# Kernel tuning notes

Measured on AMD Instinct MI355X. Metric: run time of the kernel, lower is better.

## Reference

```python
import jax, jax.numpy as jnp
import numpy as np

EMBED_DIM = 1024
NUM_HEADS = 16
HEAD_DIM = EMBED_DIM // NUM_HEADS


def setup_inputs() -> dict:
    key = jax.random.key(0)
    ks = jax.random.split(key, 11)
    B, S, E = 4, 2048, EMBED_DIM
    s = 1.0 / np.sqrt(E)
    return {
        "q": jax.random.normal(ks[0], (B, S, E), jnp.float32),
        "k": jax.random.normal(ks[1], (B, S, E), jnp.float32),
        "v": jax.random.normal(ks[2], (B, S, E), jnp.float32),
        "Wq": jax.random.uniform(ks[3], (E, E), jnp.float32, -s, s),
        "bq": jax.random.uniform(ks[4], (E,), jnp.float32, -s, s),
        "Wk": jax.random.uniform(ks[5], (E, E), jnp.float32, -s, s),
        "bk": jax.random.uniform(ks[6], (E,), jnp.float32, -s, s),
        "Wv": jax.random.uniform(ks[7], (E, E), jnp.float32, -s, s),
        "bv": jax.random.uniform(ks[8], (E,), jnp.float32, -s, s),
        "Wo": jax.random.uniform(ks[9], (E, E), jnp.float32, -s, s),
        "bo": jax.random.uniform(ks[10], (E,), jnp.float32, -s, s),
    }


def _split_heads(x):
    B, S, E = x.shape
    return x.reshape(B, S, NUM_HEADS, HEAD_DIM).transpose(0, 2, 1, 3)  # [B,H,S,D]


def reference(q, k, v, Wq, bq, Wk, bk, Wv, bv, Wo, bo):
    # torch Linear: x @ W.T + b
    Q = _split_heads(q @ Wq.T + bq)
    K = _split_heads(k @ Wk.T + bk)
    V = _split_heads(v @ Wv.T + bv)
    scale = 1.0 / jnp.sqrt(jnp.float32(HEAD_DIM))
    scores = jnp.einsum("bhqd,bhkd->bhqk", Q, K) * scale  # [B,H,S,S]
    weights = jax.nn.softmax(scores, axis=-1)
    ctx = jnp.einsum("bhqk,bhkd->bhqd", weights, V)
    B, H, S, D = ctx.shape
    merged = ctx.transpose(0, 2, 1, 3).reshape(B, S, H * D)
    out = merged @ Wo.T + bo
    return out, weights
```

## Files before the change

### kernel.cpp

```cpp
#include <hip/hip_runtime.h>
#include <hip/hip_bf16.h>

typedef __bf16 bf16x8 __attribute__((ext_vector_type(8)));
typedef float f32x4 __attribute__((ext_vector_type(4)));

constexpr size_t XQ_OFF = 0;
constexpr size_t WQ_OFF = 25165824;
constexpr size_t Q_OFF  = 29360128;
constexpr size_t KK_OFF = 37748736;
constexpr size_t VT_OFF = 46137344;
constexpr size_t CTX_OFF= 54525952;

__device__ __forceinline__ void gload16(const void* g, void* s) {
    __builtin_amdgcn_global_load_lds((__attribute__((address_space(1))) void*)g,
                                     (__attribute__((address_space(3))) void*)s, 16, 0, 0);
}
#define WAIT_VM0()   asm volatile("s_waitcnt vmcnt(0)" ::: "memory")
#define WAIT_VM4()   asm volatile("s_waitcnt vmcnt(4)" ::: "memory")
#define WAIT_VM8()   asm volatile("s_waitcnt vmcnt(8)" ::: "memory")
#define WAIT_LGKM0() asm volatile("s_waitcnt lgkmcnt(0)" ::: "memory")
#define BAR()        __builtin_amdgcn_s_barrier()

__global__ __launch_bounds__(256) void convert_k(
    const float* __restrict__ q, const float* __restrict__ k, const float* __restrict__ v,
    const float* __restrict__ Wq, const float* __restrict__ Wk, const float* __restrict__ Wv,
    const float* __restrict__ Wo, __bf16* __restrict__ ws) {
    int id = blockIdx.x * 256 + threadIdx.x;
    const int NX = 1048576;
    const int NW = 131072;
    const float* src; size_t dst; int local;
    if (id < 3 * NX) {
        int z = id / NX; local = id - z * NX;
        src = (z == 0) ? q : ((z == 1) ? k : v);
        dst = XQ_OFF + (size_t)z * 8388608;
    } else {
        int i2 = id - 3 * NX;
        int z = i2 / NW; local = i2 - z * NW;
        src = (z == 0) ? Wq : ((z == 1) ? Wk : ((z == 2) ? Wv : Wo));
        dst = WQ_OFF + (size_t)z * 1048576;
    }
    const float4* s4 = (const float4*)(src + (size_t)local * 8);
    float4 a = s4[0], b = s4[1];
    bf16x8 o;
    o[0]=(__bf16)a.x; o[1]=(__bf16)a.y; o[2]=(__bf16)a.z; o[3]=(__bf16)a.w;
    o[4]=(__bf16)b.x; o[5]=(__bf16)b.y; o[6]=(__bf16)b.z; o[7]=(__bf16)b.w;
    *(bf16x8*)(ws + dst + (size_t)local * 8) = o;
}

template<int MODE>
__global__ __launch_bounds__(256) void gemm_k(
    __bf16* __restrict__ ws,
    const float* __restrict__ bq, const float* __restrict__ bk,
    const float* __restrict__ bv, const float* __restrict__ bo,
    float* __restrict__ out) {
    const int K = 1024;
    unsigned n = blockIdx.x + 64u * (blockIdx.y + 8u * blockIdx.z);
    unsigned cpx = (MODE == 0) ? 192u : 64u;
    unsigned m_ = (n & 7u) * cpx + (n >> 3);
    unsigned bx = m_ & 63u;
    unsigned rest = m_ >> 6;
    unsigned by = rest & 7u;
    unsigned bz = rest >> 3;

    int z = (int)bz;
    const __bf16* A; const __bf16* Bm; const float* bias;
    if (MODE == 0) {
        A    = ws + XQ_OFF + (size_t)z * 8388608;
        Bm   = ws + WQ_OFF + (size_t)z * 1048576;
        bias = (z == 0) ? bq : ((z == 1) ? bk : bv);
    } else {
        A    = ws + CTX_OFF;
        Bm   = ws + WQ_OFF + (size_t)3 * 1048576;
        bias = bo;
    }
    int row0 = (int)bx * 128, col0 = (int)by * 128;
    __shared__ __align__(16) __bf16 As[2][128 * 32];
    __shared__ __align__(16) __bf16 Bs[2][128 * 32];
    int t = threadIdx.x, lane = t & 63, w = t >> 6;
    int wr = w >> 1, wc = w & 1;
    f32x4 acc[4][4];
#pragma unroll
    for (int i = 0; i < 4; ++i)
#pragma unroll
        for (int j = 0; j < 4; ++j) acc[i][j] = (f32x4){0.f, 0.f, 0.f, 0.f};

    auto stage = [&](int buf, int kt) {
#pragma unroll
        for (int i = 0; i < 2; ++i) {
            int e = ((i * 4 + w) * 64 + lane) * 8;
            int r = e >> 5, c = e & 31;
            gload16(A  + (size_t)(row0 + r) * K + kt + c, &As[buf][e]);
            gload16(Bm + (size_t)(col0 + r) * K + kt + c, &Bs[buf][e]);
        }
    };

    stage(0, 0);
    int cur = 0;
    for (int kt = 0; kt < K; kt += 32) {
        bool nx = kt + 32 < K;
        if (nx) { stage(cur ^ 1, kt + 32); WAIT_VM4(); }
        else    { WAIT_VM0(); }
        BAR();
        const __bf16* Ac = As[cur];
        const __bf16* Bc = Bs[cur];
        bf16x8 af[4], bfr[4];
#pragma unroll
        for (int f = 0; f < 4; ++f) {
            af[f]  = *(const bf16x8*)&Ac[(wr * 64 + f * 16 + (lane & 15)) * 32 + (lane >> 4) * 8];
            bfr[f] = *(const bf16x8*)&Bc[(wc * 64 + f * 16 + (lane & 15)) * 32 + (lane >> 4) * 8];
        }
#pragma unroll
        for (int fr = 0; fr < 4; ++fr)
#pragma unroll
            for (int fc = 0; fc < 4; ++fc)
                acc[fr][fc] = __builtin_amdgcn_mfma_f32_16x16x32_bf16(af[fr], bfr[fc], acc[fr][fc], 0, 0, 0);
        WAIT_LGKM0();
        BAR();
        cur ^= 1;
    }

    if (MODE == 0) {
        __bf16* dqk = ws + Q_OFF + (size_t)z * 8388608;
        __bf16* dvt = ws + VT_OFF;
#pragma unroll
        for (int fr = 0; fr < 4; ++fr)
#pragma unroll
            for (int fc = 0; fc < 4; ++fc)
#pragma unroll
                for (int r = 0; r < 4; ++r) {
                    int m = row0 + wr * 64 + fr * 16 + ((lane >> 4) << 2) + r;
                    int nn = col0 + wc * 64 + fc * 16 + (lane & 15);
                    float val = acc[fr][fc][r] + bias[nn];
                    int bb = m >> 11, s = m & 2047, h = nn >> 6, d = nn & 63;
                    size_t bh = (size_t)bb * 16 + h;
                    if (z < 2) dqk[bh * 131072 + (size_t)s * 64 + d] = (__bf16)val;
                    else       dvt[bh * 131072 + (size_t)d * 2048 + s] = (__bf16)val;
                }
    } else {
#pragma unroll
        for (int fr = 0; fr < 4; ++fr)
#pragma unroll
            for (int fc = 0; fc < 4; ++fc)
#pragma unroll
                for (int r = 0; r < 4; ++r) {
                    int m = row0 + wr * 64 + fr * 16 + ((lane >> 4) << 2) + r;
                    int nn = col0 + wc * 64 + fc * 16 + (lane & 15);
                    out[(size_t)m * 1024 + nn] = acc[fr][fc][r] + bias[nn];
                }
    }
}

__global__ __launch_bounds__(512) void rowsum_k(const __bf16* __restrict__ ws,
                                                float* __restrict__ rs_out) {
    unsigned n = blockIdx.x + 8u * blockIdx.y;
    unsigned m = (n & 7u) * 64u + (n >> 3);
    int bh = (int)(m >> 3);
    int q0 = (int)(m & 7u) * 256;
    const __bf16* Qb = ws + Q_OFF  + (size_t)bh * 131072;
    const __bf16* Kb = ws + KK_OFF + (size_t)bh * 131072;
    __shared__ __align__(16) __bf16 Ks[2][64 * 64];
    int t = threadIdx.x, lane = t & 63, w = t >> 6, g = lane >> 4;
    const float SCALE = 0.125f;

    bf16x8 aq[2][2];
#pragma unroll
    for (int f = 0; f < 2; ++f) {
        int qr = q0 + w * 32 + f * 16 + (lane & 15);
        aq[f][0] = *(const bf16x8*)&Qb[(size_t)qr * 64 + g * 8];
        aq[f][1] = *(const bf16x8*)&Qb[(size_t)qr * 64 + 32 + g * 8];
    }

    { int r = t >> 3, c8 = t & 7;
      gload16(Kb + (size_t)r * 64 + ((c8 ^ (r & 7)) << 3), &Ks[0][t * 8]); }
    WAIT_VM0(); BAR();

    float rs[8] = {0.f,0.f,0.f,0.f,0.f,0.f,0.f,0.f};
    int cur = 0;
    for (int kt = 0; kt < 2048; kt += 64) {
        bool nx = kt < 1984;
        if (nx) {
            int r = t >> 3, c8 = t & 7;
            gload16(Kb + (size_t)(kt + 64 + r) * 64 + ((c8 ^ (r & 7)) << 3), &Ks[cur ^ 1][t * 8]);
        }
        const __bf16* Kc = Ks[cur];
        __builtin_amdgcn_s_setprio(1);
#pragma unroll
        for (int kc = 0; kc < 4; ++kc) {
            int krow = kc * 16 + (lane & 15);
            bf16x8 b0 = *(const bf16x8*)((const char*)Kc + krow * 128 + ((g * 16) ^ ((krow & 7) << 4)));
            bf16x8 b1 = *(const bf16x8*)((const char*)Kc + krow * 128 + (((4 + g) * 16) ^ ((krow & 7) << 4)));
#pragma unroll
            for (int f = 0; f < 2; ++f) {
                f32x4 s = (f32x4){0.f, 0.f, 0.f, 0.f};
                s = __builtin_amdgcn_mfma_f32_16x16x32_bf16(aq[f][0], b0, s, 0, 0, 0);
                s = __builtin_amdgcn_mfma_f32_16x16x32_bf16(aq[f][1], b1, s, 0, 0, 0);
#pragma unroll
                for (int r4 = 0; r4 < 4; ++r4) rs[f * 4 + r4] += __expf(s[r4] * SCALE);
            }
        }
        __builtin_amdgcn_s_setprio(0);
        WAIT_LGKM0();
        if (nx) WAIT_VM0();
        BAR();
        cur ^= 1;
    }
#pragma unroll
    for (int msk = 1; msk < 16; msk <<= 1)
#pragma unroll
        for (int i = 0; i < 8; ++i) rs[i] += __shfl_xor(rs[i], msk);
    if ((lane & 15) == 0) {
#pragma unroll
        for (int f = 0; f < 2; ++f)
#pragma unroll
            for (int r4 = 0; r4 < 4; ++r4)
                rs_out[(size_t)bh * 2048 + q0 + w * 32 + f * 16 + g * 4 + r4] = rs[f * 4 + r4];
    }
}

__global__ __launch_bounds__(512) void attnw_k(const __bf16* __restrict__ ws,
                                               const float* __restrict__ rsf,
                                               __bf16* __restrict__ wsw,
                                               float* __restrict__ wout) {
    unsigned n = blockIdx.x + 8u * blockIdx.y;
    unsigned m = (n & 7u) * 64u + (n >> 3);
    int bh = (int)(m >> 3);
    int q0 = (int)(m & 7u) * 256;

    const __bf16* Qb = ws + Q_OFF  + (size_t)bh * 131072;
    const __bf16* Kb = ws + KK_OFF + (size_t)bh * 131072;
    const __bf16* Vb = ws + VT_OFF + (size_t)bh * 131072;
    __bf16* ctx = wsw + CTX_OFF;

    int t = threadIdx.x, lane = t & 63, w = t >> 6, g = lane >> 4;
    __shared__ __align__(16) __bf16 QP[256 * 64];
    __shared__ __align__(16) __bf16 Ks[2][64 * 64];
    __shared__ __align__(16) __bf16 Vts[2][64 * 64];
    const float SCALE = 0.125f;

    float rinv[8];
#pragma unroll
    for (int f = 0; f < 2; ++f)
#pragma unroll
        for (int r4 = 0; r4 < 4; ++r4)
            rinv[f * 4 + r4] = 1.f / rsf[(size_t)bh * 2048 + q0 + w * 32 + f * 16 + g * 4 + r4];

#pragma unroll
    for (int i = 0; i < 4; ++i) {
        int ch = t + 512 * i, r = ch >> 3, c8 = ch & 7;
        gload16(Qb + (size_t)(q0 + r) * 64 + ((c8 ^ (r & 7)) << 3), &QP[ch * 8]);
    }
    WAIT_VM0(); BAR();
    bf16x8 aq[2][2];
#pragma unroll
    for (int f = 0; f < 2; ++f) {
        int qrow = w * 32 + f * 16 + (lane & 15);
        aq[f][0] = *(const bf16x8*)((const char*)QP + qrow * 128 + ((g * 16) ^ ((qrow & 7) << 4)));
        aq[f][1] = *(const bf16x8*)((const char*)QP + qrow * 128 + (((4 + g) * 16) ^ ((qrow & 7) << 4)));
    }
    WAIT_LGKM0(); BAR();

    { int r = t >> 3, c8 = t & 7;
      gload16(Kb + (size_t)r * 64   + ((c8 ^ (r & 7)) << 3), &Ks[0][t * 8]);
      gload16(Vb + (size_t)r * 2048 + ((c8 ^ (r & 7)) << 3), &Vts[0][t * 8]); }
    WAIT_VM0(); BAR();

    f32x4 cacc[2][4];
#pragma unroll
    for (int f = 0; f < 2; ++f)
#pragma unroll
        for (int dc = 0; dc < 4; ++dc) cacc[f][dc] = (f32x4){0.f, 0.f, 0.f, 0.f};

    int cur = 0;
    for (int kt = 0; kt < 2048; kt += 64) {
        bool nx = kt < 1984;
        if (nx) {
            int r = t >> 3, c8 = t & 7;
            gload16(Kb + (size_t)(kt + 64 + r) * 64 + ((c8 ^ (r & 7)) << 3), &Ks[cur ^ 1][t * 8]);
            gload16(Vb + (size_t)r * 2048 + (kt + 64) + ((c8 ^ (r & 7)) << 3), &Vts[cur ^ 1][t * 8]);
        }
        const __bf16* Kc = Ks[cur];
        const __bf16* Vc = Vts[cur];
        __builtin_amdgcn_s_setprio(1);
#pragma unroll
        for (int kc = 0; kc < 4; ++kc) {
            int krow = kc * 16 + (lane & 15);
            bf16x8 b0 = *(const bf16x8*)((const char*)Kc + krow * 128 + ((g * 16) ^ ((krow & 7) << 4)));
            bf16x8 b1 = *(const bf16x8*)((const char*)Kc + krow * 128 + (((4 + g) * 16) ^ ((krow & 7) << 4)));
#pragma unroll
            for (int f = 0; f < 2; ++f) {
                f32x4 s = (f32x4){0.f, 0.f, 0.f, 0.f};
                s = __builtin_amdgcn_mfma_f32_16x16x32_bf16(aq[f][0], b0, s, 0, 0, 0);
                s = __builtin_amdgcn_mfma_f32_16x16x32_bf16(aq[f][1], b1, s, 0, 0, 0);
#pragma unroll
                for (int r4 = 0; r4 < 4; ++r4) {
                    float e = __expf(s[r4] * SCALE) * rinv[f * 4 + r4];
                    int prow = w * 32 + f * 16 + (g << 2) + r4;
                    int pcol = kc * 16 + (lane & 15);
                    *(__bf16*)((char*)QP + prow * 128 + ((pcol * 2) ^ ((prow & 7) << 4))) = (__bf16)e;
                }
            }
        }
        __builtin_amdgcn_s_setprio(0);
        WAIT_LGKM0();
        __builtin_amdgcn_sched_barrier(0);
        BAR();
#pragma unroll
        for (int i = 0; i < 4; ++i) {
            int ch = t + 512 * i, row = ch >> 3, c8 = ch & 7;
            bf16x8 p = *(const bf16x8*)((const char*)QP + row * 128 + ((c8 * 16) ^ ((row & 7) << 4)));
            f32x4 lo = (f32x4){(float)p[0], (float)p[1], (float)p[2], (float)p[3]};
            f32x4 hi = (f32x4){(float)p[4], (float)p[5], (float)p[6], (float)p[7]};
            float* dst = wout + ((size_t)bh * 2048 + q0 + row) * 2048 + kt + c8 * 8;
            *(f32x4*)dst = lo;
            *(f32x4*)(dst + 4) = hi;
        }
        __builtin_amdgcn_s_setprio(1);
#pragma unroll
        for (int ks = 0; ks < 2; ++ks) {
            bf16x8 ap[2];
#pragma unroll
            for (int f = 0; f < 2; ++f) {
                int arow = w * 32 + f * 16 + (lane & 15);
                ap[f] = *(const bf16x8*)((const char*)QP + arow * 128 + ((ks * 64 + g * 16) ^ ((arow & 7) << 4)));
            }
#pragma unroll
            for (int dc = 0; dc < 4; ++dc) {
                int vrow = dc * 16 + (lane & 15);
                bf16x8 bv = *(const bf16x8*)((const char*)Vc + vrow * 128 + ((ks * 64 + g * 16) ^ ((vrow & 7) << 4)));
#pragma unroll
                for (int f = 0; f < 2; ++f)
                    cacc[f][dc] = __builtin_amdgcn_mfma_f32_16x16x32_bf16(ap[f], bv, cacc[f][dc], 0, 0, 0);
            }
        }
        __builtin_amdgcn_s_setprio(0);
        WAIT_LGKM0();
        WAIT_VM8();
        BAR();
        cur ^= 1;
    }

    int bb = bh >> 4, h = bh & 15;
#pragma unroll
    for (int f = 0; f < 2; ++f)
#pragma unroll
        for (int dc = 0; dc < 4; ++dc)
#pragma unroll
            for (int r4 = 0; r4 < 4; ++r4) {
                int qg = q0 + w * 32 + f * 16 + (g << 2) + r4;
                int d = dc * 16 + (lane & 15);
                ctx[((size_t)bb * 2048 + qg) * 1024 + h * 64 + d] = (__bf16)cacc[f][dc][r4];
            }
}

extern "C" void kernel_launch(void* const* d_in, const int* in_sizes, int n_in,
                              void* d_out, int out_size, void* d_ws, size_t ws_size,
                              hipStream_t stream) {
    const float* q  = (const float*)d_in[0];
    const float* k  = (const float*)d_in[1];
    const float* v  = (const float*)d_in[2];
    const float* Wq = (const float*)d_in[3];
    const float* bq = (const float*)d_in[4];
    const float* Wk = (const float*)d_in[5];
    const float* bk = (const float*)d_in[6];
    const float* Wv = (const float*)d_in[7];
    const float* bv = (const float*)d_in[8];
    const float* Wo = (const float*)d_in[9];
    const float* bo = (const float*)d_in[10];
    __bf16* ws = (__bf16*)d_ws;
    float* out  = (float*)d_out;
    float* wout = out + 8388608;
    float* rsum = (float*)d_ws;

    convert_k<<<dim3(14336), dim3(256), 0, stream>>>(q, k, v, Wq, Wk, Wv, Wo, ws);
    gemm_k<0><<<dim3(64, 8, 3), dim3(256), 0, stream>>>(ws, bq, bk, bv, bo, out);
    rowsum_k<<<dim3(8, 64), dim3(512), 0, stream>>>(ws, rsum);
    attnw_k<<<dim3(8, 64), dim3(512), 0, stream>>>(ws, rsum, ws, wout);
    gemm_k<1><<<dim3(64, 8, 1), dim3(256), 0, stream>>>(ws, bq, bk, bv, bo, out);
}
```

Measured before the change: 542.4 us.

## Write fp32 attention weights directly from registers and load Q fragments from global

The softmax probabilities are now stored to the fp32 weights output straight from the MFMA result registers, instead of being read back from the bf16 LDS tile and re-expanded. This removes an LDS read pass per tile and writes full-precision values rather than bf16-rounded ones. The Q fragments are loaded directly from global memory into registers, dropping the LDS staging and two barriers, and the vmcnt wait is loosened to allow the many scalar stores to stay in flight. The cost is that each lane issues scattered 4-byte stores, 16 lanes per row, instead of 16-byte vector stores, which may lower write efficiency on a store-bound kernel.

```diff
diff --git a/kernel.cpp b/kernel.cpp
--- a/kernel.cpp
+++ b/kernel.cpp
@@ -17,7 +17,7 @@
 }
 #define WAIT_VM0()   asm volatile("s_waitcnt vmcnt(0)" ::: "memory")
 #define WAIT_VM4()   asm volatile("s_waitcnt vmcnt(4)" ::: "memory")
-#define WAIT_VM8()   asm volatile("s_waitcnt vmcnt(8)" ::: "memory")
+#define WAIT_VM32()  asm volatile("s_waitcnt vmcnt(32)" ::: "memory")
 #define WAIT_LGKM0() asm volatile("s_waitcnt lgkmcnt(0)" ::: "memory")
 #define BAR()        __builtin_amdgcn_s_barrier()
 
@@ -232,7 +232,7 @@
     __bf16* ctx = wsw + CTX_OFF;
 
     int t = threadIdx.x, lane = t & 63, w = t >> 6, g = lane >> 4;
-    __shared__ __align__(16) __bf16 QP[256 * 64];
+    __shared__ __align__(16) __bf16 Ps[256 * 64];
     __shared__ __align__(16) __bf16 Ks[2][64 * 64];
     __shared__ __align__(16) __bf16 Vts[2][64 * 64];
     const float SCALE = 0.125f;
@@ -244,20 +244,13 @@
         for (int r4 = 0; r4 < 4; ++r4)
             rinv[f * 4 + r4] = 1.f / rsf[(size_t)bh * 2048 + q0 + w * 32 + f * 16 + g * 4 + r4];
 
-#pragma unroll
-    for (int i = 0; i < 4; ++i) {
-        int ch = t + 512 * i, r = ch >> 3, c8 = ch & 7;
-        gload16(Qb + (size_t)(q0 + r) * 64 + ((c8 ^ (r & 7)) << 3), &QP[ch * 8]);
-    }
-    WAIT_VM0(); BAR();
     bf16x8 aq[2][2];
 #pragma unroll
     for (int f = 0; f < 2; ++f) {
-        int qrow = w * 32 + f * 16 + (lane & 15);
-        aq[f][0] = *(const bf16x8*)((const char*)QP + qrow * 128 + ((g * 16) ^ ((qrow & 7) << 4)));
-        aq[f][1] = *(const bf16x8*)((const char*)QP + qrow * 128 + (((4 + g) * 16) ^ ((qrow & 7) << 4)));
-    }
-    WAIT_LGKM0(); BAR();
+        int qr = q0 + w * 32 + f * 16 + (lane & 15);
+        aq[f][0] = *(const bf16x8*)&Qb[(size_t)qr * 64 + g * 8];
+        aq[f][1] = *(const bf16x8*)&Qb[(size_t)qr * 64 + 32 + g * 8];
+    }
 
     { int r = t >> 3, c8 = t & 7;
       gload16(Kb + (size_t)r * 64   + ((c8 ^ (r & 7)) << 3), &Ks[0][t * 8]);
@@ -291,12 +284,15 @@
                 f32x4 s = (f32x4){0.f, 0.f, 0.f, 0.f};
                 s = __builtin_amdgcn_mfma_f32_16x16x32_bf16(aq[f][0], b0, s, 0, 0, 0);
                 s = __builtin_amdgcn_mfma_f32_16x16x32_bf16(aq[f][1], b1, s, 0, 0, 0);
+                size_t wbase = ((size_t)bh * 2048 + q0 + w * 32 + f * 16 + (g << 2)) * 2048
+                               + kt + kc * 16 + (lane & 15);
 #pragma unroll
                 for (int r4 = 0; r4 < 4; ++r4) {
                     float e = __expf(s[r4] * SCALE) * rinv[f * 4 + r4];
+                    wout[wbase + (size_t)r4 * 2048] = e;
                     int prow = w * 32 + f * 16 + (g << 2) + r4;
                     int pcol = kc * 16 + (lane & 15);
-                    *(__bf16*)((char*)QP + prow * 128 + ((pcol * 2) ^ ((prow & 7) << 4))) = (__bf16)e;
+                    *(__bf16*)((char*)Ps + prow * 128 + ((pcol * 2) ^ ((prow & 7) << 4))) = (__bf16)e;
                 }
             }
         }
@@ -304,16 +300,6 @@
         WAIT_LGKM0();
         __builtin_amdgcn_sched_barrier(0);
         BAR();
-#pragma unroll
-        for (int i = 0; i < 4; ++i) {
-            int ch = t + 512 * i, row = ch >> 3, c8 = ch & 7;
-            bf16x8 p = *(const bf16x8*)((const char*)QP + row * 128 + ((c8 * 16) ^ ((row & 7) << 4)));
-            f32x4 lo = (f32x4){(float)p[0], (float)p[1], (float)p[2], (float)p[3]};
-            f32x4 hi = (f32x4){(float)p[4], (float)p[5], (float)p[6], (float)p[7]};
-            float* dst = wout + ((size_t)bh * 2048 + q0 + row) * 2048 + kt + c8 * 8;
-            *(f32x4*)dst = lo;
-            *(f32x4*)(dst + 4) = hi;
-        }
         __builtin_amdgcn_s_setprio(1);
 #pragma unroll
         for (int ks = 0; ks < 2; ++ks) {
@@ -321,7 +307,7 @@
 #pragma unroll
             for (int f = 0; f < 2; ++f) {
                 int arow = w * 32 + f * 16 + (lane & 15);
-                ap[f] = *(const bf16x8*)((const char*)QP + arow * 128 + ((ks * 64 + g * 16) ^ ((arow & 7) << 4)));
+                ap[f] = *(const bf16x8*)((const char*)Ps + arow * 128 + ((ks * 64 + g * 16) ^ ((arow & 7) << 4)));
             }
 #pragma unroll
             for (int dc = 0; dc < 4; ++dc) {
@@ -334,7 +320,7 @@
         }
         __builtin_amdgcn_s_setprio(0);
         WAIT_LGKM0();
-        WAIT_VM8();
+        WAIT_VM32();
         BAR();
         cur ^= 1;
     }
```

Result: slower. 558.1 us (+2.9%).
